# Optimization experiments

Measured on AMD Instinct MI355X. Metric: run time of the kernel, lower is better.

## Reference

```python
import jax, jax.numpy as jnp
import numpy as np

N, IN_CAPS, IN_LEN = 32, 1152, 32
OUT_CAPS, OUT_LEN = 64, 32
NUM_ITERATIONS = 3


def setup_inputs() -> dict:
    key = jax.random.key(0)
    k1, k2 = jax.random.split(key)
    x = jax.random.normal(k1, (N, IN_CAPS, IN_LEN), dtype=jnp.float32)
    # learnable weight, torch.randn init: (out_capsules, out_length, in_length)
    weight = jax.random.normal(k2, (OUT_CAPS, OUT_LEN, IN_LEN), dtype=jnp.float32)
    return {"x": x, "weight": weight}


def _squash(v):
    # v * ||v|| / (1 + ||v||^2)  ==  (||v||^2/(1+||v||^2)) * v/||v||
    norm_sq = jnp.sum(v * v, axis=-1, keepdims=True)
    norm = jnp.sqrt(norm_sq)
    return v * norm / (1.0 + norm_sq)


def reference(x, weight):
    # priors u_hat: [N, out_caps, in_caps, out_len]
    priors = jnp.einsum('oli,bni->bonl', weight, x)
    logits = jnp.zeros_like(priors)
    output = None
    for r in range(NUM_ITERATIONS):
        # coupling coefficients: softmax over output capsules (axis=1)
        probs = jax.nn.softmax(logits, axis=1)
        # weighted sum over input capsules -> [N, out_caps, 1, out_len]
        output = jnp.sum(probs * priors, axis=-2, keepdims=True)
        if r != NUM_ITERATIONS - 1:
            output = _squash(output)
            # agreement update: [N, out_caps, in_caps, 1]
            logits = logits + jnp.sum(priors * output, axis=-1, keepdims=True)
    output = _squash(output)  # squash=True default
    return jnp.squeeze(output, axis=-2)  # [N, out_caps, out_len]
```

## Files before the change

### kernel.cpp

```cpp
#include <hip/hip_runtime.h>
#include <math.h>


#define N_B      32
#define IN_CAPS  1152
#define IN_LEN   32
#define OUT_CAPS 64
#define OUT_LEN  32

#define NCHUNK 16
#define NPB    (IN_CAPS / NCHUNK)
#define PASS_WAVES 4
#define NPW    (NPB / PASS_WAVES)
#define TSTR   36

#define DPPV(v, ctrl) \
    __int_as_float(__builtin_amdgcn_update_dpp(0, __float_as_int(v), ctrl, 0xF, 0xF, true))

__device__ __forceinline__ float wave_max(float v) {
    v = fmaxf(v, DPPV(v, 0xB1));
    v = fmaxf(v, DPPV(v, 0x4E));
    v = fmaxf(v, DPPV(v, 0x141));
    v = fmaxf(v, DPPV(v, 0x140));
    v = fmaxf(v, __shfl_xor(v, 16, 64));
    v = fmaxf(v, __shfl_xor(v, 32, 64));
    return v;
}
__device__ __forceinline__ float wave_sum(float v) {
    v += DPPV(v, 0xB1);
    v += DPPV(v, 0x4E);
    v += DPPV(v, 0x141);
    v += DPPV(v, 0x140);
    v += __shfl_xor(v, 16, 64);
    v += __shfl_xor(v, 32, 64);
    return v;
}

__device__ __forceinline__ void pass_and_flush(const float* __restrict__ x,
                                               const float* T_lds, float* buf,
                                               float* __restrict__ part,
                                               int b, int c, int tid, int lane, int wave) {
    float t[IN_LEN];
    {
#pragma unroll
        for (int q = 0; q < 8; ++q) {
            const float4 v = *(const float4*)&T_lds[lane * TSTR + q * 4];
            t[4 * q] = v.x; t[4 * q + 1] = v.y; t[4 * q + 2] = v.z; t[4 * q + 3] = v.w;
        }
    }
    asm volatile("" : "+v"(t[0]), "+v"(t[1]), "+v"(t[2]), "+v"(t[3]),
                      "+v"(t[4]), "+v"(t[5]), "+v"(t[6]), "+v"(t[7]),
                      "+v"(t[8]), "+v"(t[9]), "+v"(t[10]), "+v"(t[11]),
                      "+v"(t[12]), "+v"(t[13]), "+v"(t[14]), "+v"(t[15]));
    asm volatile("" : "+v"(t[16]), "+v"(t[17]), "+v"(t[18]), "+v"(t[19]),
                      "+v"(t[20]), "+v"(t[21]), "+v"(t[22]), "+v"(t[23]),
                      "+v"(t[24]), "+v"(t[25]), "+v"(t[26]), "+v"(t[27]),
                      "+v"(t[28]), "+v"(t[29]), "+v"(t[30]), "+v"(t[31]));

    float s[IN_LEN];
#pragma unroll
    for (int i = 0; i < IN_LEN; ++i) s[i] = 0.f;

    const float* xw = x + ((size_t)b * IN_CAPS + c * NPB + wave * NPW) * IN_LEN;

#define L4(acc, R, k) \
    acc = fmaf((R).x, t[k],     acc); acc = fmaf((R).y, t[k + 1], acc); \
    acc = fmaf((R).z, t[k + 2], acc); acc = fmaf((R).w, t[k + 3], acc);
#define S4(R, k) \
    s[k]     = fmaf(prob, (R).x, s[k]);     s[k + 1] = fmaf(prob, (R).y, s[k + 1]); \
    s[k + 2] = fmaf(prob, (R).z, s[k + 2]); s[k + 3] = fmaf(prob, (R).w, s[k + 3]);

#pragma unroll
    for (int j = 0; j < NPW; ++j) {
        const float4* xr = (const float4*)(xw + j * IN_LEN);
        const float4 r0 = xr[0], r1 = xr[1], r2 = xr[2], r3 = xr[3],
                     r4 = xr[4], r5 = xr[5], r6 = xr[6], r7 = xr[7];

        float l0 = 0.f, l1 = 0.f, l2 = 0.f, l3 = 0.f;
        L4(l0, r0, 0)  L4(l1, r1, 4)  L4(l2, r2, 8)  L4(l3, r3, 12)
        L4(l0, r4, 16) L4(l1, r5, 20) L4(l2, r6, 24) L4(l3, r7, 28)
        const float logit = (l0 + l1) + (l2 + l3);

        const float m = wave_max(logit);
        const float p = __expf(logit - m);
        const float S = wave_sum(p);
        const float prob = p * __builtin_amdgcn_rcpf(S);

        S4(r0, 0)  S4(r1, 4)  S4(r2, 8)  S4(r3, 12)
        S4(r4, 16) S4(r5, 20) S4(r6, 24) S4(r7, 28)
    }
#undef L4
#undef S4

    {
        float4* dst = (float4*)&buf[(wave * OUT_CAPS + lane) * TSTR];
#pragma unroll
        for (int q = 0; q < 8; ++q)
            dst[q] = make_float4(s[4 * q], s[4 * q + 1], s[4 * q + 2], s[4 * q + 3]);
    }
    __syncthreads();
    {
        float4* pb4 = (float4*)(part + ((size_t)b * NCHUNK + c) * OUT_CAPS * IN_LEN);
        for (int e = tid; e < OUT_CAPS * IN_LEN / 4; e += 256) {
            const int o = e >> 3, q4 = (e & 7) * 4;
            const float4 a0 = *(const float4*)&buf[(0 * OUT_CAPS + o) * TSTR + q4];
            const float4 a1 = *(const float4*)&buf[(1 * OUT_CAPS + o) * TSTR + q4];
            const float4 a2 = *(const float4*)&buf[(2 * OUT_CAPS + o) * TSTR + q4];
            const float4 a3 = *(const float4*)&buf[(3 * OUT_CAPS + o) * TSTR + q4];
            pb4[e] = make_float4(a0.x + a1.x + a2.x + a3.x,
                                 a0.y + a1.y + a2.y + a3.y,
                                 a0.z + a1.z + a2.z + a3.z,
                                 a0.w + a1.w + a2.w + a3.w);
        }
    }
}

__global__ __launch_bounds__(256, 2) void kA(const float* __restrict__ x,
                                             const float* __restrict__ W,
                                             float* __restrict__ T,
                                             float* __restrict__ part) {
    const int b    = blockIdx.x >> 4;
    const int c    = blockIdx.x & (NCHUNK - 1);
    const int tid  = threadIdx.x;
    const int lane = tid & 63;
    const int wave = __builtin_amdgcn_readfirstlane(tid >> 6);

    __shared__ __align__(16) float T_lds[OUT_CAPS * TSTR];
    __shared__ __align__(16) float buf[PASS_WAVES * OUT_CAPS * TSTR];

    {
        float4* red4 = (float4*)buf;
        const int q = tid & 7, g = tid >> 3;
        const float* xb = x + (size_t)b * IN_CAPS * IN_LEN;
        float4 acc = make_float4(0.f, 0.f, 0.f, 0.f);
        for (int n = g; n < IN_CAPS; n += 32) {
            const float4 v = *(const float4*)(xb + n * IN_LEN + q * 4);
            acc.x += v.x; acc.y += v.y; acc.z += v.z; acc.w += v.w;
        }
        red4[g * 8 + q] = acc;
    }
    __syncthreads();
    float* u     = buf + 1024;
    float* scale = buf + 3072;
    float* s0    = buf + 3136;
    if (tid < 8) {
        const float4* red4 = (const float4*)buf;
        float4 v = make_float4(0.f, 0.f, 0.f, 0.f);
        for (int g = 0; g < 32; ++g) {
            const float4 r = red4[g * 8 + tid];
            v.x += r.x; v.y += r.y; v.z += r.z; v.w += r.w;
        }
        const float inv = 1.f / 64.f;
        s0[tid * 4 + 0] = v.x * inv;
        s0[tid * 4 + 1] = v.y * inv;
        s0[tid * 4 + 2] = v.z * inv;
        s0[tid * 4 + 3] = v.w * inv;
    }
    __syncthreads();

    for (int e = tid; e < OUT_CAPS * OUT_LEN; e += 256) {
        const float* wrow = W + (size_t)e * IN_LEN;
        float a = 0.f;
#pragma unroll
        for (int i = 0; i < IN_LEN; ++i) a = fmaf(wrow[i], s0[i], a);
        u[e] = a;
    }
    __syncthreads();
    if (tid < OUT_CAPS) {
        float ns = 0.f;
#pragma unroll
        for (int l = 0; l < OUT_LEN; ++l) { const float v = u[tid * OUT_LEN + l]; ns = fmaf(v, v, ns); }
        scale[tid] = sqrtf(ns) / (1.f + ns);
    }
    __syncthreads();
    for (int e = tid; e < OUT_CAPS * IN_LEN; e += 256) {
        const int o = e >> 5, i = e & 31;
        float a = 0.f;
#pragma unroll
        for (int l = 0; l < OUT_LEN; ++l)
            a = fmaf(W[((size_t)o * OUT_LEN + l) * IN_LEN + i], u[o * OUT_LEN + l], a);
        T_lds[o * TSTR + i] = a * scale[o];
    }
    __syncthreads();

    if (c == 0) {
        for (int e = tid; e < OUT_CAPS * IN_LEN; e += 256)
            T[(size_t)b * OUT_CAPS * IN_LEN + e] = T_lds[(e >> 5) * TSTR + (e & 31)];
    }

    pass_and_flush(x, T_lds, buf, part, b, c, tid, lane, wave);
}

__global__ __launch_bounds__(256, 2) void kB(const float* __restrict__ x,
                                             const float* __restrict__ W,
                                             const float* __restrict__ T,
                                             float* __restrict__ part) {
    const int b    = blockIdx.x >> 4;
    const int c    = blockIdx.x & (NCHUNK - 1);
    const int tid  = threadIdx.x;
    const int lane = tid & 63;
    const int wave = __builtin_amdgcn_readfirstlane(tid >> 6);

    __shared__ __align__(16) float T_lds[OUT_CAPS * TSTR];
    __shared__ __align__(16) float buf[PASS_WAVES * OUT_CAPS * TSTR];

    float* s_lds = buf;
    float* uu    = buf + 2048;
    float* sc    = buf + 4096;

    {
        const float4* pb4 = (const float4*)(part + (size_t)b * NCHUNK * OUT_CAPS * IN_LEN);
        for (int e = tid; e < OUT_CAPS * IN_LEN / 4; e += 256) {
            float4 acc = make_float4(0.f, 0.f, 0.f, 0.f);
#pragma unroll
            for (int cc = 0; cc < NCHUNK; ++cc) {
                const float4 v = pb4[cc * (OUT_CAPS * IN_LEN / 4) + e];
                acc.x += v.x; acc.y += v.y; acc.z += v.z; acc.w += v.w;
            }
            ((float4*)s_lds)[e] = acc;
        }
    }
    __syncthreads();
    for (int e = tid; e < OUT_CAPS * OUT_LEN; e += 256) {
        const int o = e >> 5;
        const float* wrow = W + (size_t)e * IN_LEN;
        const float* srow = s_lds + o * IN_LEN;
        float a = 0.f;
#pragma unroll
        for (int i = 0; i < IN_LEN; ++i) a = fmaf(wrow[i], srow[i], a);
        uu[e] = a;
    }
    __syncthreads();
    if (tid < OUT_CAPS) {
        float ns = 0.f;
#pragma unroll
        for (int l = 0; l < OUT_LEN; ++l) { const float v = uu[tid * OUT_LEN + l]; ns = fmaf(v, v, ns); }
        sc[tid] = sqrtf(ns) / (1.f + ns);
    }
    __syncthreads();

    for (int e = tid; e < OUT_CAPS * IN_LEN; e += 256) {
        const int o = e >> 5, i = e & 31;
        float a = 0.f;
#pragma unroll
        for (int l = 0; l < OUT_LEN; ++l)
            a = fmaf(W[((size_t)o * OUT_LEN + l) * IN_LEN + i], uu[o * OUT_LEN + l], a);
        T_lds[o * TSTR + i] = T[(size_t)b * OUT_CAPS * IN_LEN + e] + a * sc[o];
    }
    __syncthreads();

    pass_and_flush(x, T_lds, buf, part, b, c, tid, lane, wave);
}

__global__ __launch_bounds__(256) void kC(const float* __restrict__ W,
                                          const float* __restrict__ part,
                                          float* __restrict__ out) {
    const int b   = blockIdx.x >> 3;
    const int og  = blockIdx.x & 7;
    const int tid = threadIdx.x;
    const int ol  = tid >> 5;
    const int i   = tid & 31;
    const int o   = og * 8 + ol;

    float a = 0.f;
    const float* pb = part + (size_t)b * NCHUNK * OUT_CAPS * IN_LEN + o * IN_LEN + i;
#pragma unroll
    for (int cc = 0; cc < NCHUNK; ++cc) a += pb[cc * OUT_CAPS * IN_LEN];

    __shared__ float s_lds[8][33];
    s_lds[ol][i] = a;
    __syncthreads();

    const float* wrow = W + ((size_t)o * OUT_LEN + i) * IN_LEN;
    float u = 0.f;
#pragma unroll
    for (int k = 0; k < IN_LEN; ++k) u = fmaf(wrow[k], s_lds[ol][k], u);

    float ns = u * u;
    ns += __shfl_xor(ns, 1, 64);
    ns += __shfl_xor(ns, 2, 64);
    ns += __shfl_xor(ns, 4, 64);
    ns += __shfl_xor(ns, 8, 64);
    ns += __shfl_xor(ns, 16, 64);
    const float scale = sqrtf(ns) / (1.f + ns);

    out[((size_t)b * OUT_CAPS + o) * OUT_LEN + i] = u * scale;
}

extern "C" void kernel_launch(void* const* d_in, const int* in_sizes, int n_in,
                              void* d_out, int out_size, void* d_ws, size_t ws_size,
                              hipStream_t stream) {
    const float* x = (const float*)d_in[0];
    const float* W = (const float*)d_in[1];
    float* out = (float*)d_out;

    float* T    = (float*)d_ws;
    float* part = T + (size_t)N_B * OUT_CAPS * IN_LEN;

    kA<<<N_B * NCHUNK, 256, 0, stream>>>(x, W, T, part);
    kB<<<N_B * NCHUNK, 256, 0, stream>>>(x, W, T, part);
    kC<<<N_B * 8,      256, 0, stream>>>(W, part, out);
}
```

Measured before the change: 142.3 us.

## Split first-iteration setup into per-batch init kernel and remap block order

Before, each of the 16 chunk blocks per batch recomputed the mean of x, the W·s0 product and T. That setup now runs once per batch in a new k_init kernel that writes T to global memory, and a lean k_pass1 kernel reads T rows directly. Block indices are remapped so consecutive blocks spread across batches, likely for better L2 or XCD locality. The second pass writes to a separate partial buffer so it no longer overwrites the one it reads. The cost is an extra kernel launch with only 32 blocks on the critical path, plus more workspace.

Result: faster. 130.0 us (-8.6%).

```diff
diff --git a/kernel.cpp b/kernel.cpp
--- a/kernel.cpp
+++ b/kernel.cpp
@@ -13,6 +13,11 @@
 #define PASS_WAVES 4
 #define NPW    (NPB / PASS_WAVES)
 #define TSTR   36
+
+#define DECODE_BC(d, b, c) \
+    const int _slot = (d) >> 3; \
+    const int b = ((d) & 7) * 4 + (_slot >> 4); \
+    const int c = _slot & 15;
 
 #define DPPV(v, ctrl) \
     __int_as_float(__builtin_amdgcn_update_dpp(0, __float_as_int(v), ctrl, 0xF, 0xF, true))
@@ -37,14 +42,15 @@
 }
 
 __device__ __forceinline__ void pass_and_flush(const float* __restrict__ x,
-                                               const float* T_lds, float* buf,
-                                               float* __restrict__ part,
+                                               const float* T_row_src, int t_stride,
+                                               float* buf,
+                                               float* __restrict__ part_out,
                                                int b, int c, int tid, int lane, int wave) {
     float t[IN_LEN];
     {
 #pragma unroll
         for (int q = 0; q < 8; ++q) {
-            const float4 v = *(const float4*)&T_lds[lane * TSTR + q * 4];
+            const float4 v = *(const float4*)&T_row_src[lane * t_stride + q * 4];
             t[4 * q] = v.x; t[4 * q + 1] = v.y; t[4 * q + 2] = v.z; t[4 * q + 3] = v.w;
         }
     }
@@ -100,7 +106,7 @@
     }
     __syncthreads();
     {
-        float4* pb4 = (float4*)(part + ((size_t)b * NCHUNK + c) * OUT_CAPS * IN_LEN);
+        float4* pb4 = (float4*)(part_out + ((size_t)b * NCHUNK + c) * OUT_CAPS * IN_LEN);
         for (int e = tid; e < OUT_CAPS * IN_LEN / 4; e += 256) {
             const int o = e >> 3, q4 = (e & 7) * 4;
             const float4 a0 = *(const float4*)&buf[(0 * OUT_CAPS + o) * TSTR + q4];
@@ -115,39 +121,30 @@
     }
 }
 
-__global__ __launch_bounds__(256, 2) void kA(const float* __restrict__ x,
-                                             const float* __restrict__ W,
-                                             float* __restrict__ T,
-                                             float* __restrict__ part) {
-    const int b    = blockIdx.x >> 4;
-    const int c    = blockIdx.x & (NCHUNK - 1);
-    const int tid  = threadIdx.x;
-    const int lane = tid & 63;
-    const int wave = __builtin_amdgcn_readfirstlane(tid >> 6);
-
-    __shared__ __align__(16) float T_lds[OUT_CAPS * TSTR];
-    __shared__ __align__(16) float buf[PASS_WAVES * OUT_CAPS * TSTR];
-
-    {
-        float4* red4 = (float4*)buf;
-        const int q = tid & 7, g = tid >> 3;
-        const float* xb = x + (size_t)b * IN_CAPS * IN_LEN;
+__global__ __launch_bounds__(256) void k_init(const float* __restrict__ x,
+                                              const float* __restrict__ W,
+                                              float* __restrict__ T) {
+    const int b   = blockIdx.x;
+    const int tid = threadIdx.x;
+    const float* xb = x + (size_t)b * IN_CAPS * IN_LEN;
+
+    __shared__ float4 red4[32][8];
+    {
+        const int q = tid & 7;
+        const int g = tid >> 3;
         float4 acc = make_float4(0.f, 0.f, 0.f, 0.f);
         for (int n = g; n < IN_CAPS; n += 32) {
             const float4 v = *(const float4*)(xb + n * IN_LEN + q * 4);
             acc.x += v.x; acc.y += v.y; acc.z += v.z; acc.w += v.w;
         }
-        red4[g * 8 + q] = acc;
-    }
-    __syncthreads();
-    float* u     = buf + 1024;
-    float* scale = buf + 3072;
-    float* s0    = buf + 3136;
+        red4[g][q] = acc;
+    }
+    __syncthreads();
+    __shared__ float s0[IN_LEN];
     if (tid < 8) {
-        const float4* red4 = (const float4*)buf;
         float4 v = make_float4(0.f, 0.f, 0.f, 0.f);
         for (int g = 0; g < 32; ++g) {
-            const float4 r = red4[g * 8 + tid];
+            const float4 r = red4[g][tid];
             v.x += r.x; v.y += r.y; v.z += r.z; v.w += r.w;
         }
         const float inv = 1.f / 64.f;
@@ -158,6 +155,7 @@
     }
     __syncthreads();
 
+    __shared__ float u[OUT_CAPS * OUT_LEN];
     for (int e = tid; e < OUT_CAPS * OUT_LEN; e += 256) {
         const float* wrow = W + (size_t)e * IN_LEN;
         float a = 0.f;
@@ -166,6 +164,8 @@
         u[e] = a;
     }
     __syncthreads();
+
+    __shared__ float scale[OUT_CAPS];
     if (tid < OUT_CAPS) {
         float ns = 0.f;
 #pragma unroll
@@ -173,30 +173,37 @@
         scale[tid] = sqrtf(ns) / (1.f + ns);
     }
     __syncthreads();
+
     for (int e = tid; e < OUT_CAPS * IN_LEN; e += 256) {
         const int o = e >> 5, i = e & 31;
         float a = 0.f;
 #pragma unroll
         for (int l = 0; l < OUT_LEN; ++l)
             a = fmaf(W[((size_t)o * OUT_LEN + l) * IN_LEN + i], u[o * OUT_LEN + l], a);
-        T_lds[o * TSTR + i] = a * scale[o];
-    }
-    __syncthreads();
-
-    if (c == 0) {
-        for (int e = tid; e < OUT_CAPS * IN_LEN; e += 256)
-            T[(size_t)b * OUT_CAPS * IN_LEN + e] = T_lds[(e >> 5) * TSTR + (e & 31)];
-    }
-
-    pass_and_flush(x, T_lds, buf, part, b, c, tid, lane, wave);
+        T[(size_t)b * OUT_CAPS * IN_LEN + e] = a * scale[o];
+    }
+}
+
+__global__ __launch_bounds__(256, 2) void k_pass1(const float* __restrict__ x,
+                                                  const float* __restrict__ T,
+                                                  float* __restrict__ part) {
+    DECODE_BC(blockIdx.x, b, c)
+    const int tid  = threadIdx.x;
+    const int lane = tid & 63;
+    const int wave = __builtin_amdgcn_readfirstlane(tid >> 6);
+
+    __shared__ __align__(16) float buf[PASS_WAVES * OUT_CAPS * TSTR];
+
+    pass_and_flush(x, T + (size_t)b * OUT_CAPS * IN_LEN, IN_LEN,
+                   buf, part, b, c, tid, lane, wave);
 }
 
 __global__ __launch_bounds__(256, 2) void kB(const float* __restrict__ x,
                                              const float* __restrict__ W,
                                              const float* __restrict__ T,
-                                             float* __restrict__ part) {
-    const int b    = blockIdx.x >> 4;
-    const int c    = blockIdx.x & (NCHUNK - 1);
+                                             const float* __restrict__ part,
+                                             float* __restrict__ part2) {
+    DECODE_BC(blockIdx.x, b, c)
     const int tid  = threadIdx.x;
     const int lane = tid & 63;
     const int wave = __builtin_amdgcn_readfirstlane(tid >> 6);
@@ -249,11 +256,11 @@
     }
     __syncthreads();
 
-    pass_and_flush(x, T_lds, buf, part, b, c, tid, lane, wave);
+    pass_and_flush(x, T_lds, TSTR, buf, part2, b, c, tid, lane, wave);
 }
 
 __global__ __launch_bounds__(256) void kC(const float* __restrict__ W,
-                                          const float* __restrict__ part,
+                                          const float* __restrict__ part2,
                                           float* __restrict__ out) {
     const int b   = blockIdx.x >> 3;
     const int og  = blockIdx.x & 7;
@@ -263,7 +270,7 @@
     const int o   = og * 8 + ol;
 
     float a = 0.f;
-    const float* pb = part + (size_t)b * NCHUNK * OUT_CAPS * IN_LEN + o * IN_LEN + i;
+    const float* pb = part2 + (size_t)b * NCHUNK * OUT_CAPS * IN_LEN + o * IN_LEN + i;
 #pragma unroll
     for (int cc = 0; cc < NCHUNK; ++cc) a += pb[cc * OUT_CAPS * IN_LEN];
 
@@ -294,10 +301,12 @@
     const float* W = (const float*)d_in[1];
     float* out = (float*)d_out;
 
-    float* T    = (float*)d_ws;
-    float* part = T + (size_t)N_B * OUT_CAPS * IN_LEN;
-
-    kA<<<N_B * NCHUNK, 256, 0, stream>>>(x, W, T, part);
-    kB<<<N_B * NCHUNK, 256, 0, stream>>>(x, W, T, part);
-    kC<<<N_B * 8,      256, 0, stream>>>(W, part, out);
-}
+    float* T     = (float*)d_ws;
+    float* part  = T + (size_t)N_B * OUT_CAPS * IN_LEN;
+    float* part2 = part + (size_t)N_B * NCHUNK * OUT_CAPS * IN_LEN;
+
+    k_init <<<N_B,          256, 0, stream>>>(x, W, T);
+    k_pass1<<<N_B * NCHUNK, 256, 0, stream>>>(x, T, part);
+    kB     <<<N_B * NCHUNK, 256, 0, stream>>>(x, W, T, part, part2);
+    kC     <<<N_B * 8,      256, 0, stream>>>(W, part2, out);
+}
```
